# Optimization experiments

Measured on AMD Instinct MI355X. Metric: run time of the kernel, lower is better.

Reference implementation:

```python
import jax, jax.numpy as jnp
import numpy as np

K = 4  # top-k from init
BN_IS_FOLDED = True  # BatchNorm (eval mode) folded into per-channel scale s and shift t


def tconv(x, W):
    # x: (b, C, v, n); W: (Cout, Cin, 3) temporal conv, kernel (3,1,1), padding (1,0,0), no bias
    return jax.lax.conv_general_dilated(
        x, W[:, :, :, None], window_strides=(1, 1),
        padding=((1, 1), (0, 0)), dimension_numbers=('NCHW', 'OIHW', 'NCHW'))


def gcn_single(xn, src, dst, Wg, bg):
    # PyG GCNConv: add self-loops, symmetric normalization, then scatter-add.
    N = xn.shape[0]
    xl = xn @ Wg  # (N, C)
    loop = jnp.arange(N, dtype=src.dtype)
    s = jnp.concatenate([src, loop])
    d = jnp.concatenate([dst, loop])
    deg = jax.ops.segment_sum(jnp.ones(s.shape[0], dtype=xn.dtype), d, num_segments=N)
    dinv = jnp.where(deg > 0, jax.lax.rsqrt(deg), 0.0)
    norm = dinv[s] * dinv[d]
    out = jax.ops.segment_sum(norm[:, None] * xl[s], d, num_segments=N)
    return out + bg


def setup_inputs() -> dict:
    key = jax.random.key(0)
    ks = jax.random.split(key, 10)
    C = 256
    x = jax.random.normal(ks[0], (512, C, 16, 16), dtype=jnp.float32)
    Wd = jax.random.normal(ks[1], (C, C, 3), dtype=jnp.float32) * 0.02
    s1 = 1.0 + 0.1 * jax.random.normal(ks[2], (C,), dtype=jnp.float32)
    t1 = 0.1 * jax.random.normal(ks[3], (C,), dtype=jnp.float32)
    Wg = jax.random.normal(ks[4], (C, C), dtype=jnp.float32) * 0.02
    bg = 0.01 * jax.random.normal(ks[5], (C,), dtype=jnp.float32)
    Wu = jax.random.normal(ks[6], (C, C, 3), dtype=jnp.float32) * 0.02
    s2 = 1.0 + 0.1 * jax.random.normal(ks[7], (C,), dtype=jnp.float32)
    t2 = 0.1 * jax.random.normal(ks[8], (C,), dtype=jnp.float32)
    return {"x": x, "batch": 4, "Wd": Wd, "s1": s1, "t1": t1,
            "Wg": Wg, "bg": bg, "Wu": Wu, "s2": s2, "t2": t2}


def reference(x, batch, Wd, s1, t1, Wg, bg, Wu, s2, t2):
    tlen, c, h, w = x.shape
    b = batch
    v = tlen // b
    hw = h * w
    # (tlen,c,h,w) -> (b,c,v,h*w)
    x4 = x.reshape(b, v, c, h, w).transpose(0, 2, 1, 3, 4).reshape(b, c, v, hw)
    xd = tconv(x4, Wd) * s1[None, :, None, None] + t1[None, :, None, None]  # down_conv + BN(eval)

    # --- dynamic graph build (no-grad in original) ---
    f = jax.lax.stop_gradient(xd).transpose(0, 2, 3, 1)  # (b, v, hw, c)
    f1, f2 = f[:, :-1], f[:, 1:]                          # (b, t_1, hw, c)
    t_1 = v - 1
    sq1 = jnp.sum(f1 * f1, axis=-1)                       # (b,t_1,hw)
    sq2 = jnp.sum(f2 * f2, axis=-1)
    dots = jnp.einsum('btnc,btmc->btnm', f1, f2)
    d2 = jnp.maximum(sq1[..., :, None] + sq2[..., None, :] - 2.0 * dots, 0.0)
    sim = -jnp.sqrt(d2).reshape(b, t_1, hw * hw)
    sim = sim / jnp.maximum(jnp.linalg.norm(sim, axis=-1, keepdims=True), 1e-12)  # F.normalize
    sim = jnp.where(sim < 0.05, 100.0, sim)
    _, idx = jax.lax.top_k(sim, K)                        # (b, t_1, K)
    frame = jnp.arange(t_1, dtype=jnp.int32)[None, :, None]
    row = (idx // hw).astype(jnp.int32) + frame * hw
    col = (idx % hw).astype(jnp.int32) + (frame + 1) * hw
    row = row.reshape(b, -1)
    col = col.reshape(b, -1)
    src = jnp.concatenate([row, col], axis=1)             # forward + reversed edges
    dst = jnp.concatenate([col, row], axis=1)

    # --- per-sample GCN (batched with vmap) ---
    nodes = xd.transpose(0, 2, 3, 1).reshape(b, v * hw, c)  # 'b c v n -> b (v n) c'
    out = jax.vmap(lambda xn, s, d: gcn_single(xn, s, d, Wg, bg))(nodes, src, dst)

    # --- up path ---
    o4 = out.transpose(0, 2, 1).reshape(b, c, v, hw)
    xu = tconv(o4, Wu) * s2[None, :, None, None] + t2[None, :, None, None]
    return xu.reshape(b, c, v, h, w).transpose(0, 2, 1, 3, 4).reshape(tlen, c, h, w)
```

## Files before the change

kernel.cpp:

```cpp
#include <hip/hip_runtime.h>

typedef __attribute__((ext_vector_type(8))) short short8;
typedef __attribute__((ext_vector_type(4))) float f32x4;
typedef unsigned short u16;
typedef unsigned int u32;

#define FENCE() asm volatile("" ::: "memory")

__device__ __forceinline__ void gld_lds16(const void* g, void* l) {
  __builtin_amdgcn_global_load_lds((const __attribute__((address_space(1))) void*)g,
                                   (__attribute__((address_space(3))) void*)l,
                                   16, 0, 0);
}

__device__ __forceinline__ u16 f2b(float x) {
  union { float f; u32 u; } v; v.f = x;
  u32 u = v.u;
  return (u16)((u + 0x7FFFu + ((u >> 16) & 1u)) >> 16);
}
__device__ __forceinline__ float b2f(u16 x) {
  union { u32 u; float f; } v; v.u = ((u32)x) << 16; return v.f;
}
__device__ __forceinline__ u32 pack_pair(float lo, float hi) {
  return (u32)f2b(lo) | ((u32)f2b(hi) << 16);
}

__global__ __launch_bounds__(256) void k_prep(const float* __restrict__ Wd, const float* __restrict__ Wg,
                                              const float* __restrict__ Wu,
                                              const float* __restrict__ s1, const float* __restrict__ t1,
                                              const float* __restrict__ bg,
                                              u16* __restrict__ WdT, u16* __restrict__ Wup,
                                              u16* __restrict__ WgS,
                                              float* __restrict__ c0, float* __restrict__ tWg) {
  int blk = blockIdx.x;
  int tid = threadIdx.x;
  if (blk == 1024) {
    int j = tid;
    float a = 0.f;
    for (int co = 0; co < 256; ++co) a += t1[co] * Wg[co * 256 + j];
    tWg[j] = a;
    c0[j] = a + bg[j];
    return;
  }
  int id = blk * 256 + tid;
  if (id < 196608) {
    int kk = id >> 16;
    int rem = id & 65535;
    int a = rem >> 8, b = rem & 255;
    Wup[id] = f2b(Wu[(u32)a * 768 + (u32)b * 3 + kk]);
    WdT[id] = f2b(Wd[(u32)b * 768 + (u32)a * 3 + kk]);
  } else {
    int id2 = id - 196608;
    int j = id2 >> 8, co = id2 & 255;
    WgS[id2] = f2b(Wg[co * 256 + j] * s1[co]);
  }
}

__global__ __launch_bounds__(256) void k_zero(u16* __restrict__ outz, u16* __restrict__ xTz) {
  int gid = blockIdx.x * 256 + threadIdx.x;
  int i = gid * 8;
  int buf = (i >= 327680) ? 1 : 0;
  int wi = i - buf * 327680;
  int f = wi >> 16;
  int off = wi & 65535;
  u16* dst = (buf ? xTz : outz) + (size_t)f * 129 * 65536 + off;
  *(uint4*)dst = make_uint4(0u, 0u, 0u, 0u);
}

__global__ __launch_bounds__(256) void k_transpose(const float* __restrict__ x, u16* __restrict__ xTz) {
  __shared__ u16 tile[64][72];
  int blk = blockIdx.x;
  int tl = blk >> 4;
  int sub = blk & 15;
  int ci0 = (sub >> 2) << 6;
  int p0 = (sub & 3) << 6;
  int tid = threadIdx.x;
  int i = tid >> 2;
  int ch = tid & 3;
  const float* gsrc = x + (size_t)tl * 65536 + (ci0 + i) * 256 + p0 + ch * 16;
  __align__(16) u16 cv[16];
#pragma unroll
  for (int v4 = 0; v4 < 4; ++v4) {
    float4 f = *(const float4*)(gsrc + v4 * 4);
    cv[v4 * 4 + 0] = f2b(f.x);
    cv[v4 * 4 + 1] = f2b(f.y);
    cv[v4 * 4 + 2] = f2b(f.z);
    cv[v4 * 4 + 3] = f2b(f.w);
  }
  *(uint4*)&tile[i][ch * 16] = *(const uint4*)&cv[0];
  *(uint4*)&tile[i][ch * 16 + 8] = *(const uint4*)&cv[8];
  __syncthreads();
  __align__(16) u16 tmp[16];
#pragma unroll
  for (int cc = 0; cc < 16; ++cc) tmp[cc] = tile[ch * 16 + cc][i];
  int fi = (tl >> 7) * 129 + (tl & 127) + 1;
  u16* gdst = xTz + (size_t)fi * 65536 + (p0 + i) * 256 + ci0 + ch * 16;
  *(uint4*)(gdst) = *(const uint4*)&tmp[0];
  *(uint4*)(gdst + 8) = *(const uint4*)&tmp[8];
}

__device__ __forceinline__ void stage_tile(const u16* __restrict__ g, int ldg, u16* s, int w, int lane) {
  int r = lane >> 2;
  int cc = (lane & 3) * 8;
#pragma unroll
  for (int j = 0; j < 2; ++j) {
    gld_lds16(g + (w * 32 + j * 16 + r) * ldg + cc, s + (w * 32 + j * 16) * 32);
  }
}

__device__ __forceinline__ void mfma_tiles(const u16* sA, const u16* sB, f32x4 acc[4][4],
                                           int wr, int wc, int lane) {
  int m16 = lane & 15;
  int q8 = (lane >> 4) * 8;
  short8 a[4], b[4];
#pragma unroll
  for (int mi = 0; mi < 4; ++mi) a[mi] = *(const short8*)(sA + (wr * 64 + mi * 16 + m16) * 32 + q8);
#pragma unroll
  for (int ni = 0; ni < 4; ++ni) b[ni] = *(const short8*)(sB + (wc * 64 + ni * 16 + m16) * 32 + q8);
#pragma unroll
  for (int mi = 0; mi < 4; ++mi)
#pragma unroll
    for (int ni = 0; ni < 4; ++ni)
      acc[mi][ni] = __builtin_amdgcn_mfma_f32_16x16x32_bf16(a[mi], b[ni], acc[mi][ni], 0, 0, 0);
}

__device__ __forceinline__ void store_pairs(u16* base, int row0, int stride, int colb,
                                            const float v[4], bool ev) {
  float pv[4];
#pragma unroll
  for (int r = 0; r < 4; ++r) pv[r] = __shfl_xor(v[r], 1, 64);
  u32 wd0 = ev ? pack_pair(v[0], pv[0]) : pack_pair(pv[0], v[0]);
  u32 wd1 = ev ? pack_pair(v[1], pv[1]) : pack_pair(pv[1], v[1]);
  u32 wd2 = ev ? pack_pair(v[2], pv[2]) : pack_pair(pv[2], v[2]);
  u32 wd3 = ev ? pack_pair(v[3], pv[3]) : pack_pair(pv[3], v[3]);
  u32 wa = ev ? wd0 : wd2;
  u32 wb = ev ? wd1 : wd3;
  int rs = ev ? 0 : 2;
  *(u32*)(base + (size_t)(row0 + rs) * stride + colb) = wa;
  *(u32*)(base + (size_t)(row0 + rs + 1) * stride + colb) = wb;
}

__device__ __forceinline__ void store_pairs_f32(float* base, int row0, int stride, int colb,
                                                const float v[4], bool ev) {
  float pv[4];
#pragma unroll
  for (int r = 0; r < 4; ++r) pv[r] = __shfl_xor(v[r], 1, 64);
  float2 wa, wb;
  if (ev) { wa = make_float2(v[0], pv[0]); wb = make_float2(v[1], pv[1]); }
  else    { wa = make_float2(pv[2], v[2]); wb = make_float2(pv[3], v[3]); }
  int rs = ev ? 0 : 2;
  *(float2*)(base + (size_t)(row0 + rs) * stride + colb) = wa;
  *(float2*)(base + (size_t)(row0 + rs + 1) * stride + colb) = wb;
}

__global__ __launch_bounds__(256) void k_wcomb(const u16* __restrict__ WgS, const u16* __restrict__ WdT,
                                               u16* __restrict__ Wcomb) {
  __shared__ u16 sA[128 * 32];
  __shared__ u16 sB[128 * 32];
  int blk = blockIdx.x;
  int kk = blk >> 2;
  int tile = blk & 3;
  int tm = tile >> 1, tn = tile & 1;
  int tid = threadIdx.x, lane = tid & 63, w = tid >> 6;
  int wr = w >> 1, wc = w & 1;
  f32x4 acc[4][4];
#pragma unroll
  for (int i = 0; i < 4; ++i)
#pragma unroll
    for (int j = 0; j < 4; ++j) acc[i][j] = (f32x4){0.f, 0.f, 0.f, 0.f};
  const u16* gA = WgS + (size_t)(tm * 128) * 256;
  const u16* gB = WdT + (size_t)kk * 65536 + (size_t)(tn * 128) * 256;
  for (int ks = 0; ks < 8; ++ks) {
    stage_tile(gA + ks * 32, 256, sA, w, lane);
    stage_tile(gB + ks * 32, 256, sB, w, lane);
    __syncthreads();
    mfma_tiles(sA, sB, acc, wr, wc, lane);
    __syncthreads();
  }
  int q = lane >> 4, c = lane & 15;
  bool ev = (lane & 1) == 0;
  u16* obase = Wcomb + (size_t)kk * 65536;
#pragma unroll
  for (int mi = 0; mi < 4; ++mi) {
    int row0 = tm * 128 + wr * 64 + mi * 16 + q * 4;
#pragma unroll
    for (int ni = 0; ni < 4; ++ni) {
      float v[4];
#pragma unroll
      for (int r = 0; r < 4; ++r) v[r] = acc[mi][ni][r];
      int colb = tn * 128 + wc * 64 + ni * 16 + (c & ~1);
      store_pairs(obase, row0, 256, colb, v, ev);
    }
  }
}


__device__ __forceinline__ void stage_part(int s, const u16* Ab, const u16* Bb,
                                           u16* sA, u16* sB, int wuni, int g0) {
  if (s >= 48) return;
  const int tau = s >> 2;
  const int pt = s & 3;
  const int toff = ((tau >> 2) << 16) + ((tau & 3) << 6);
  const int half = pt & 1;
  const u16* src = ((pt & 2) ? Ab : Bb) + toff + (half << 15) + g0;
  u16* dst = ((pt & 2) ? sA : sB) + ((tau & 1) << 14) + (half << 13) + wuni;
  gld_lds16(src, dst);
  gld_lds16(src + 16384, dst + 4096);
}

template<int QUAD, int NH>
__device__ __forceinline__ void mfma_quad(f32x4 (&acc)[8][4], const short8 (&af)[2][4],
                                          const short8 (&bf)[2][2][2]) {
#pragma unroll
  for (int k = 0; k < 2; ++k)
#pragma unroll
    for (int m = 0; m < 4; ++m)
#pragma unroll
      for (int nj = 0; nj < 2; ++nj)
        acc[QUAD * 4 + m][NH * 2 + nj] = __builtin_amdgcn_mfma_f32_16x16x32_bf16(
            af[k][m], bf[NH][k][nj], acc[QUAD * 4 + m][NH * 2 + nj], 0, 0, 0);
}

__device__ __forceinline__ void gemm256_core(const u16* __restrict__ Ab, const u16* __restrict__ Bb,
                                             u16* sA, u16* sB, int tid, f32x4 (&acc)[8][4]) {
  const int lane = tid & 63;
  const int w = tid >> 6;
  const int wr = w >> 2;
  const int wc = w & 3;
  const int m16 = lane & 15;
  const int xorm = (lane & 7) << 4;
  const int q16b = (lane >> 4) << 4;
  const int koffe0 = ((q16b) ^ xorm) >> 1;
  const int koffe1 = ((64 + q16b) ^ xorm) >> 1;
  const int srow = tid >> 3;
  const int scol = ((tid & 7) ^ (srow & 7)) << 3;
  const int g0 = srow * 256 + scol;
  const int wuni = w << 9;

#pragma unroll
  for (int i = 0; i < 8; ++i)
#pragma unroll
    for (int j = 0; j < 4; ++j) acc[i][j] = (f32x4){0.f, 0.f, 0.f, 0.f};

#pragma unroll
  for (int s = 0; s < 7; ++s) stage_part(s, Ab, Bb, sA, sB, wuni, g0);
  asm volatile("s_waitcnt vmcnt(6)" ::: "memory");
  __builtin_amdgcn_s_barrier();
  FENCE();

  short8 af[2][4];
  short8 bf[2][2][2];
#pragma unroll 2
  for (int kt = 0; kt < 12; ++kt) {
    const int cb = kt & 1;
    const u16* aH = sA + cb * 16384 + wr * 8192;
    const u16* bH = sB + cb * 16384 + (wc >> 1) * 8192;
    const int bR0 = (wc & 1) << 6;
#pragma unroll
    for (int m = 0; m < 4; ++m) {
      const u16* p = aH + (m * 16 + m16) * 64;
      af[0][m] = *(const short8*)(p + koffe0);
      af[1][m] = *(const short8*)(p + koffe1);
    }
#pragma unroll
    for (int nh = 0; nh < 2; ++nh)
#pragma unroll
      for (int nj = 0; nj < 2; ++nj) {
        const u16* p = bH + (bR0 + (nh * 2 + nj) * 16 + m16) * 64;
        bf[nh][0][nj] = *(const short8*)(p + koffe0);
        bf[nh][1][nj] = *(const short8*)(p + koffe1);
      }
    stage_part(4 * kt + 7, Ab, Bb, sA, sB, wuni, g0);
    FENCE();
    __builtin_amdgcn_s_barrier();
    FENCE();
    __builtin_amdgcn_s_setprio(1);
    mfma_quad<0, 0>(acc, af, bf);
    __builtin_amdgcn_s_setprio(0);
    FENCE();
    __builtin_amdgcn_s_barrier();
    FENCE();
    stage_part(4 * kt + 8, Ab, Bb, sA, sB, wuni, g0);
    FENCE();
    __builtin_amdgcn_s_barrier();
    FENCE();
    __builtin_amdgcn_s_setprio(1);
    mfma_quad<0, 1>(acc, af, bf);
    __builtin_amdgcn_s_setprio(0);
    FENCE();
    __builtin_amdgcn_s_barrier();
    FENCE();
#pragma unroll
    for (int m = 0; m < 4; ++m) {
      const u16* p = aH + (64 + m * 16 + m16) * 64;
      af[0][m] = *(const short8*)(p + koffe0);
      af[1][m] = *(const short8*)(p + koffe1);
    }
    stage_part(4 * kt + 9, Ab, Bb, sA, sB, wuni, g0);
    FENCE();
    __builtin_amdgcn_s_barrier();
    FENCE();
    __builtin_amdgcn_s_setprio(1);
    mfma_quad<1, 0>(acc, af, bf);
    __builtin_amdgcn_s_setprio(0);
    FENCE();
    __builtin_amdgcn_s_barrier();
    FENCE();
    stage_part(4 * kt + 10, Ab, Bb, sA, sB, wuni, g0);
    FENCE();
    __builtin_amdgcn_s_barrier();
    FENCE();
    __builtin_amdgcn_s_setprio(1);
    mfma_quad<1, 1>(acc, af, bf);
    __builtin_amdgcn_s_setprio(0);
    if (kt < 10) asm volatile("s_waitcnt vmcnt(6)" ::: "memory");
    else         asm volatile("s_waitcnt vmcnt(0)" ::: "memory");
    __builtin_amdgcn_s_barrier();
    FENCE();
  }
}

__global__ __launch_bounds__(512, 2) void k_g12(const u16* __restrict__ xTz, const u16* __restrict__ Wcomb,
                                                const float* __restrict__ c0, const float* __restrict__ tWg,
                                                u16* __restrict__ outz, float* __restrict__ edge) {
  __shared__ u16 sA[32768];
  __shared__ u16 sB[32768];
  int bsw = (int)blockIdx.x;
  int bt = (bsw & 7) * 64 + (bsw >> 3);
  int b = bt >> 7, t = bt & 127;
  int tid = threadIdx.x;
  const u16* Ab = xTz + (size_t)(b * 129 + t) * 65536;
  const u16* Bb = Wcomb;
  f32x4 acc[8][4];
  gemm256_core(Ab, Bb, sA, sB, tid, acc);

  int lane = tid & 63, w = tid >> 6, wr = w >> 2, wc = w & 3;
  int q = lane >> 4, cc16 = lane & 15;
  bool ev = (lane & 1) == 0;
  float c0v[4], tWgv[4];
#pragma unroll
  for (int ni = 0; ni < 4; ++ni) {
    int j = wc * 64 + ni * 16 + cc16;
    c0v[ni] = c0[j];
    tWgv[ni] = tWg[j];
  }
  u16* obase = outz + (size_t)(b * 129 + t + 1) * 65536;
#pragma unroll
  for (int mi = 0; mi < 8; ++mi) {
    int row0 = wr * 128 + mi * 16 + q * 4;
#pragma unroll
    for (int ni = 0; ni < 4; ++ni) {
      float v[4];
#pragma unroll
      for (int r = 0; r < 4; ++r) v[r] = acc[mi][ni][r] + c0v[ni];
      store_pairs(obase, row0, 256, wc * 64 + ni * 16 + (cc16 & ~1), v, ev);
    }
  }
  if (wr == 0 && q == 0) {
    float* eb = edge + (size_t)bt * 1024;
#pragma unroll
    for (int ni = 0; ni < 4; ++ni) {
      float vE[4];
#pragma unroll
      for (int r = 0; r < 4; ++r) vE[r] = acc[0][ni][r] + tWgv[ni];
      store_pairs_f32(eb, 0, 256, wc * 64 + ni * 16 + (cc16 & ~1), vE, ev);
    }
  }
}

__device__ __forceinline__ float dinv0(int t) {
  if (t == 0) return 0.44721359549995793f;
  if (t == 127) return 0.7071067811865476f;
  return 0.4082482904638631f;
}
__global__ __launch_bounds__(256) void k_fix(const float* __restrict__ edge, const float* __restrict__ bg,
                                             u16* __restrict__ outz) {
  int bt = blockIdx.x;
  int b = bt >> 7;
  int t = bt & 127;
  int j = threadIdx.x;
  const float ISQ2 = 0.7071067811865476f;
  float bgv = bg[j];
  float e_t = edge[(size_t)bt * 1024 + j];
  float At = dinv0(t);
  float o0 = bgv + At * At * e_t;
  if (t <= 126) {
    float At1 = dinv0(t + 1);
    const float* en = edge + (size_t)(bt + 1) * 1024;
    float s = At1 * en[j] + ISQ2 * (en[256 + j] + en[512 + j] + en[768 + j]);
    o0 += At * s;
  }
  float em1 = 0.f, Atm1 = 0.f;
  if (t >= 1) {
    Atm1 = dinv0(t - 1);
    em1 = edge[(size_t)(bt - 1) * 1024 + j];
    o0 += At * Atm1 * em1;
  }
  u16* ob = outz + (size_t)(b * 129 + t + 1) * 65536;
  ob[j] = f2b(o0);
#pragma unroll
  for (int k = 1; k <= 3; ++k) {
    float m = edge[(size_t)bt * 1024 + k * 256 + j];
    float ok = (t == 0) ? (bgv + m) : (bgv + 0.5f * m + ISQ2 * Atm1 * em1);
    ob[k * 256 + j] = f2b(ok);
  }
}

__global__ __launch_bounds__(512, 2) void k_g3(const u16* __restrict__ outz, const u16* __restrict__ Wup,
                                               const float* __restrict__ s2, const float* __restrict__ t2,
                                               float* __restrict__ y) {
  __shared__ u16 sA[32768];
  __shared__ u16 sB[32768];
  int bsw = (int)blockIdx.x;
  int bt = (bsw & 7) * 64 + (bsw >> 3);
  int b = bt >> 7, t = bt & 127;
  int tid = threadIdx.x;
  const u16* Ab = Wup;
  const u16* Bb = outz + (size_t)(b * 129 + t) * 65536;
  f32x4 acc[8][4];
  gemm256_core(Ab, Bb, sA, sB, tid, acc);

  int lane = tid & 63, w = tid >> 6, wr = w >> 2, wc = w & 3;
  int q = lane >> 4, cc16 = lane & 15;
  bool ev = (lane & 1) == 0;
  float* ybase = y + (size_t)bt * 65536;
#pragma unroll
  for (int mi = 0; mi < 8; ++mi) {
    int rl = wr * 128 + mi * 16 + q * 4;
    float4 s4 = *(const float4*)(s2 + rl);
    float4 t4 = *(const float4*)(t2 + rl);
#pragma unroll
    for (int ni = 0; ni < 4; ++ni) {
      float v[4];
      v[0] = acc[mi][ni][0] * s4.x + t4.x;
      v[1] = acc[mi][ni][1] * s4.y + t4.y;
      v[2] = acc[mi][ni][2] * s4.z + t4.z;
      v[3] = acc[mi][ni][3] * s4.w + t4.w;
      store_pairs_f32(ybase, rl, 256, wc * 64 + ni * 16 + (cc16 & ~1), v, ev);
    }
  }
}

extern "C" void kernel_launch(void* const* d_in, const int* in_sizes, int n_in,
                              void* d_out, int out_size, void* d_ws, size_t ws_size,
                              hipStream_t stream) {
  (void)in_sizes; (void)n_in; (void)out_size; (void)ws_size;
  const float* x  = (const float*)d_in[0];
  const float* Wd = (const float*)d_in[2];
  const float* s1 = (const float*)d_in[3];
  const float* t1 = (const float*)d_in[4];
  const float* Wg = (const float*)d_in[5];
  const float* bg = (const float*)d_in[6];
  const float* Wu = (const float*)d_in[7];
  const float* s2 = (const float*)d_in[8];
  const float* t2 = (const float*)d_in[9];
  float* y = (float*)d_out;
  char* ws = (char*)d_ws;
  u16*   outz  = (u16*)(ws);
  u16*   xTz   = (u16*)(ws + 67764224);
  u16*   WdT   = (u16*)(ws + 135528448);
  u16*   WgS   = (u16*)(ws + 135921664);
  u16*   Wup   = (u16*)(ws + 136052736);
  u16*   Wcomb = (u16*)(ws + 136445952);
  float* c0    = (float*)(ws + 136839168);
  float* tWg   = (float*)(ws + 136840192);
  float* edge  = (float*)d_out;

  k_prep<<<dim3(1025), dim3(256), 0, stream>>>(Wd, Wg, Wu, s1, t1, bg, WdT, Wup, WgS, c0, tWg);
  k_wcomb<<<dim3(12), dim3(256), 0, stream>>>(WgS, WdT, Wcomb);
  k_zero<<<dim3(320), dim3(256), 0, stream>>>(outz, xTz);
  k_transpose<<<dim3(8192), dim3(256), 0, stream>>>(x, xTz);
  k_g12<<<dim3(512), dim3(512), 0, stream>>>(xTz, Wcomb, c0, tWg, outz, edge);
  k_fix<<<dim3(512), dim3(256), 0, stream>>>(edge, bg, outz);
  k_g3<<<dim3(512), dim3(512), 0, stream>>>(outz, Wup, s2, t2, y);
}
```

Measured before the change: 398.4 us.

## Merge prep, wcomb, zero and transpose into one kernel with scalar Wcomb

```diff
diff --git a/kernel.cpp b/kernel.cpp
--- a/kernel.cpp
+++ b/kernel.cpp
@@ -25,56 +25,77 @@
   return (u32)f2b(lo) | ((u32)f2b(hi) << 16);
 }
 
-__global__ __launch_bounds__(256) void k_prep(const float* __restrict__ Wd, const float* __restrict__ Wg,
-                                              const float* __restrict__ Wu,
-                                              const float* __restrict__ s1, const float* __restrict__ t1,
-                                              const float* __restrict__ bg,
-                                              u16* __restrict__ WdT, u16* __restrict__ Wup,
-                                              u16* __restrict__ WgS,
-                                              float* __restrict__ c0, float* __restrict__ tWg) {
+__global__ __launch_bounds__(256) void k_pre(const float* __restrict__ x,
+                                             const float* __restrict__ Wd, const float* __restrict__ Wg,
+                                             const float* __restrict__ Wu,
+                                             const float* __restrict__ s1, const float* __restrict__ t1,
+                                             const float* __restrict__ bg,
+                                             u16* __restrict__ xTz, u16* __restrict__ outz,
+                                             u16* __restrict__ Wup, u16* __restrict__ Wcomb,
+                                             float* __restrict__ c0, float* __restrict__ tWg) {
+  __shared__ u16 tile[64][72];
   int blk = blockIdx.x;
   int tid = threadIdx.x;
-  if (blk == 1024) {
+  if (blk < 768) {
+    int kk = blk >> 8;
+    int ci = blk & 255;
     int j = tid;
-    float a = 0.f;
-    for (int co = 0; co < 256; ++co) a += t1[co] * Wg[co * 256 + j];
+    float a0 = 0.f, a1 = 0.f, a2 = 0.f, a3 = 0.f;
+    for (int co = 0; co < 256; co += 4) {
+      float w0 = b2f(f2b(Wg[(co + 0) * 256 + j] * s1[co + 0]));
+      float w1 = b2f(f2b(Wg[(co + 1) * 256 + j] * s1[co + 1]));
+      float w2 = b2f(f2b(Wg[(co + 2) * 256 + j] * s1[co + 2]));
+      float w3 = b2f(f2b(Wg[(co + 3) * 256 + j] * s1[co + 3]));
+      float d0 = b2f(f2b(Wd[(u32)(co + 0) * 768 + (u32)ci * 3 + kk]));
+      float d1 = b2f(f2b(Wd[(u32)(co + 1) * 768 + (u32)ci * 3 + kk]));
+      float d2 = b2f(f2b(Wd[(u32)(co + 2) * 768 + (u32)ci * 3 + kk]));
+      float d3 = b2f(f2b(Wd[(u32)(co + 3) * 768 + (u32)ci * 3 + kk]));
+      a0 = fmaf(w0, d0, a0);
+      a1 = fmaf(w1, d1, a1);
+      a2 = fmaf(w2, d2, a2);
+      a3 = fmaf(w3, d3, a3);
+    }
+    Wcomb[(size_t)kk * 65536 + (size_t)j * 256 + ci] = f2b((a0 + a1) + (a2 + a3));
+    return;
+  }
+  if (blk == 768) {
+    int j = tid;
+    float a0 = 0.f, a1 = 0.f, a2 = 0.f, a3 = 0.f;
+    for (int co = 0; co < 256; co += 4) {
+      a0 = fmaf(t1[co + 0], Wg[(co + 0) * 256 + j], a0);
+      a1 = fmaf(t1[co + 1], Wg[(co + 1) * 256 + j], a1);
+      a2 = fmaf(t1[co + 2], Wg[(co + 2) * 256 + j], a2);
+      a3 = fmaf(t1[co + 3], Wg[(co + 3) * 256 + j], a3);
+    }
+    float a = (a0 + a1) + (a2 + a3);
     tWg[j] = a;
     c0[j] = a + bg[j];
     return;
   }
-  int id = blk * 256 + tid;
-  if (id < 196608) {
+  if (blk < 1537) {
+    int id = (blk - 769) * 256 + tid;
     int kk = id >> 16;
     int rem = id & 65535;
     int a = rem >> 8, b = rem & 255;
     Wup[id] = f2b(Wu[(u32)a * 768 + (u32)b * 3 + kk]);
-    WdT[id] = f2b(Wd[(u32)b * 768 + (u32)a * 3 + kk]);
-  } else {
-    int id2 = id - 196608;
-    int j = id2 >> 8, co = id2 & 255;
-    WgS[id2] = f2b(Wg[co * 256 + j] * s1[co]);
-  }
-}
-
-__global__ __launch_bounds__(256) void k_zero(u16* __restrict__ outz, u16* __restrict__ xTz) {
-  int gid = blockIdx.x * 256 + threadIdx.x;
-  int i = gid * 8;
-  int buf = (i >= 327680) ? 1 : 0;
-  int wi = i - buf * 327680;
-  int f = wi >> 16;
-  int off = wi & 65535;
-  u16* dst = (buf ? xTz : outz) + (size_t)f * 129 * 65536 + off;
-  *(uint4*)dst = make_uint4(0u, 0u, 0u, 0u);
-}
-
-__global__ __launch_bounds__(256) void k_transpose(const float* __restrict__ x, u16* __restrict__ xTz) {
-  __shared__ u16 tile[64][72];
-  int blk = blockIdx.x;
-  int tl = blk >> 4;
-  int sub = blk & 15;
+    return;
+  }
+  if (blk < 1857) {
+    int gid = (blk - 1537) * 256 + tid;
+    int i = gid * 8;
+    int buf = (i >= 327680) ? 1 : 0;
+    int wi = i - buf * 327680;
+    int f = wi >> 16;
+    int off = wi & 65535;
+    u16* dst = (buf ? xTz : outz) + (size_t)f * 129 * 65536 + off;
+    *(uint4*)dst = make_uint4(0u, 0u, 0u, 0u);
+    return;
+  }
+  int tblk = blk - 1857;
+  int tl = tblk >> 4;
+  int sub = tblk & 15;
   int ci0 = (sub >> 2) << 6;
   int p0 = (sub & 3) << 6;
-  int tid = threadIdx.x;
   int i = tid >> 2;
   int ch = tid & 3;
   const float* gsrc = x + (size_t)tl * 65536 + (ci0 + i) * 256 + p0 + ch * 16;
@@ -97,31 +118,6 @@
   u16* gdst = xTz + (size_t)fi * 65536 + (p0 + i) * 256 + ci0 + ch * 16;
   *(uint4*)(gdst) = *(const uint4*)&tmp[0];
   *(uint4*)(gdst + 8) = *(const uint4*)&tmp[8];
-}
-
-__device__ __forceinline__ void stage_tile(const u16* __restrict__ g, int ldg, u16* s, int w, int lane) {
-  int r = lane >> 2;
-  int cc = (lane & 3) * 8;
-#pragma unroll
-  for (int j = 0; j < 2; ++j) {
-    gld_lds16(g + (w * 32 + j * 16 + r) * ldg + cc, s + (w * 32 + j * 16) * 32);
-  }
-}
-
-__device__ __forceinline__ void mfma_tiles(const u16* sA, const u16* sB, f32x4 acc[4][4],
-                                           int wr, int wc, int lane) {
-  int m16 = lane & 15;
-  int q8 = (lane >> 4) * 8;
-  short8 a[4], b[4];
-#pragma unroll
-  for (int mi = 0; mi < 4; ++mi) a[mi] = *(const short8*)(sA + (wr * 64 + mi * 16 + m16) * 32 + q8);
-#pragma unroll
-  for (int ni = 0; ni < 4; ++ni) b[ni] = *(const short8*)(sB + (wc * 64 + ni * 16 + m16) * 32 + q8);
-#pragma unroll
-  for (int mi = 0; mi < 4; ++mi)
-#pragma unroll
-    for (int ni = 0; ni < 4; ++ni)
-      acc[mi][ni] = __builtin_amdgcn_mfma_f32_16x16x32_bf16(a[mi], b[ni], acc[mi][ni], 0, 0, 0);
 }
 
 __device__ __forceinline__ void store_pairs(u16* base, int row0, int stride, int colb,
@@ -151,47 +147,6 @@
   int rs = ev ? 0 : 2;
   *(float2*)(base + (size_t)(row0 + rs) * stride + colb) = wa;
   *(float2*)(base + (size_t)(row0 + rs + 1) * stride + colb) = wb;
-}
-
-__global__ __launch_bounds__(256) void k_wcomb(const u16* __restrict__ WgS, const u16* __restrict__ WdT,
-                                               u16* __restrict__ Wcomb) {
-  __shared__ u16 sA[128 * 32];
-  __shared__ u16 sB[128 * 32];
-  int blk = blockIdx.x;
-  int kk = blk >> 2;
-  int tile = blk & 3;
-  int tm = tile >> 1, tn = tile & 1;
-  int tid = threadIdx.x, lane = tid & 63, w = tid >> 6;
-  int wr = w >> 1, wc = w & 1;
-  f32x4 acc[4][4];
-#pragma unroll
-  for (int i = 0; i < 4; ++i)
-#pragma unroll
-    for (int j = 0; j < 4; ++j) acc[i][j] = (f32x4){0.f, 0.f, 0.f, 0.f};
-  const u16* gA = WgS + (size_t)(tm * 128) * 256;
-  const u16* gB = WdT + (size_t)kk * 65536 + (size_t)(tn * 128) * 256;
-  for (int ks = 0; ks < 8; ++ks) {
-    stage_tile(gA + ks * 32, 256, sA, w, lane);
-    stage_tile(gB + ks * 32, 256, sB, w, lane);
-    __syncthreads();
-    mfma_tiles(sA, sB, acc, wr, wc, lane);
-    __syncthreads();
-  }
-  int q = lane >> 4, c = lane & 15;
-  bool ev = (lane & 1) == 0;
-  u16* obase = Wcomb + (size_t)kk * 65536;
-#pragma unroll
-  for (int mi = 0; mi < 4; ++mi) {
-    int row0 = tm * 128 + wr * 64 + mi * 16 + q * 4;
-#pragma unroll
-    for (int ni = 0; ni < 4; ++ni) {
-      float v[4];
-#pragma unroll
-      for (int r = 0; r < 4; ++r) v[r] = acc[mi][ni][r];
-      int colb = tn * 128 + wc * 64 + ni * 16 + (c & ~1);
-      store_pairs(obase, row0, 256, colb, v, ev);
-    }
-  }
 }
 
 
@@ -458,18 +413,13 @@
   char* ws = (char*)d_ws;
   u16*   outz  = (u16*)(ws);
   u16*   xTz   = (u16*)(ws + 67764224);
-  u16*   WdT   = (u16*)(ws + 135528448);
-  u16*   WgS   = (u16*)(ws + 135921664);
   u16*   Wup   = (u16*)(ws + 136052736);
   u16*   Wcomb = (u16*)(ws + 136445952);
   float* c0    = (float*)(ws + 136839168);
   float* tWg   = (float*)(ws + 136840192);
   float* edge  = (float*)d_out;
 
-  k_prep<<<dim3(1025), dim3(256), 0, stream>>>(Wd, Wg, Wu, s1, t1, bg, WdT, Wup, WgS, c0, tWg);
-  k_wcomb<<<dim3(12), dim3(256), 0, stream>>>(WgS, WdT, Wcomb);
-  k_zero<<<dim3(320), dim3(256), 0, stream>>>(outz, xTz);
-  k_transpose<<<dim3(8192), dim3(256), 0, stream>>>(x, xTz);
+  k_pre<<<dim3(10049), dim3(256), 0, stream>>>(x, Wd, Wg, Wu, s1, t1, bg, xTz, outz, Wup, Wcomb, c0, tWg);
   k_g12<<<dim3(512), dim3(512), 0, stream>>>(xTz, Wcomb, c0, tWg, outz, edge);
   k_fix<<<dim3(512), dim3(256), 0, stream>>>(edge, bg, outz);
   k_g3<<<dim3(512), dim3(512), 0, stream>>>(outz, Wup, s2, t2, y);
```

Result: no change. 405.9 us (+1.9%).
